# Optimization experiments

Measured on AMD Instinct MI355X. Metric: run time of the kernel, lower is better.

## Reference

```python
import jax, jax.numpy as jnp
import numpy as np

LN_EPS = 1e-5   # torch nn.LayerNorm default
R_EPS = 1e-8    # eps used in log(R.clamp(min=eps))


def layernorm(x, g, b):
    mu = jnp.mean(x, axis=-1, keepdims=True)
    var = jnp.var(x, axis=-1, keepdims=True)
    return (x - mu) * jax.lax.rsqrt(var + LN_EPS) * g + b


def setup_inputs() -> dict:
    S, B, C, h, w, d = 4, 1, 128, 10, 10, 10
    nL = 2  # num_layers
    key = jax.random.key(0)
    ks = jax.random.split(key, 20)
    std = 0.02
    inp = {
        "z": jax.random.normal(ks[0], (S, B, C, h, w, d), jnp.float32),
        "r": jax.random.uniform(ks[1], (S,), jnp.float32, 0.1, 1.0),
        "seq_embed": std * jax.random.normal(ks[2], (S, C), jnp.float32),
        # per-layer attention params, stacked on leading layer axis
        "Wq": std * jax.random.normal(ks[3], (nL, C, C), jnp.float32),
        "Wk": std * jax.random.normal(ks[4], (nL, C, C), jnp.float32),
        "Wv": std * jax.random.normal(ks[5], (nL, C, C), jnp.float32),
        "Wp": std * jax.random.normal(ks[6], (nL, C, C), jnp.float32),
        "beta": jnp.ones((nL,), jnp.float32),
        "ln1_g": jnp.ones((nL, C), jnp.float32),
        "ln1_b": jnp.zeros((nL, C), jnp.float32),
        # FFN params
        "ffn_w1": std * jax.random.normal(ks[7], (C, 4 * C), jnp.float32),
        "ffn_b1": jnp.zeros((4 * C,), jnp.float32),
        "ffn_w2": std * jax.random.normal(ks[8], (4 * C, C), jnp.float32),
        "ffn_b2": jnp.zeros((C,), jnp.float32),
        "ln2_g": jnp.ones((C,), jnp.float32),
        "ln2_b": jnp.zeros((C,), jnp.float32),
    }
    return inp


def _forward(z, r, seq_embed, Wq, Wk, Wv, Wp, beta, ln1_g, ln1_b,
             ffn_w1, ffn_b1, ffn_w2, ffn_b2, ln2_g, ln2_b):
    S, B, C, h, w, d = z.shape
    N = h * w * d
    L = S * N
    nL, _, _ = Wq.shape
    H = 8
    Dh = C // H
    scale = Dh ** (-0.5)

    # tokenize: [S,B,C,h,w,d] -> [B, S*N, C] with per-sequence embedding added
    tokens = z.reshape(S, B, C, N).transpose(1, 0, 3, 2)      # [B,S,N,C]
    tokens = tokens + seq_embed[None, :, None, :]
    tokens = tokens.reshape(B, L, C)

    # reliability bias: log(clamp(outer(r_tok, r_tok), eps))  [L,L]
    r_tok = jnp.repeat(r, N)                                   # [L]
    log_R = jnp.log(jnp.clip(r_tok[:, None] * r_tok[None, :], R_EPS, None))

    for l in range(nL):
        residual = tokens
        Q = (tokens @ Wq[l]).reshape(B, L, H, Dh)
        K = (tokens @ Wk[l]).reshape(B, L, H, Dh)
        V = (tokens @ Wv[l]).reshape(B, L, H, Dh)
        attn = jnp.einsum('bihd,bjhd->bhij', Q, K) * scale     # [B,H,L,L]
        attn = attn + beta[l] * log_R[None, None]
        attn = jax.nn.softmax(attn, axis=-1)
        out = jnp.einsum('bhij,bjhd->bihd', attn, V).reshape(B, L, C)
        out = out @ Wp[l]
        tokens = layernorm(out + residual, ln1_g[l], ln1_b[l])

    # FFN (exact GELU, matching torch nn.GELU default) + residual + LN
    hdn = jax.nn.gelu(tokens @ ffn_w1 + ffn_b1, approximate=False)
    tokens = layernorm((hdn @ ffn_w2 + ffn_b2) + tokens, ln2_g, ln2_b)

    # de-tokenize: [B,L,C] -> [B, S*C, h, w, d]
    tokens = tokens.reshape(B, S, N, C).transpose(0, 1, 3, 2)  # [B,S,C,N]
    return tokens.reshape(B, S * C, h, w, d)


def reference(z, r, seq_embed, Wq, Wk, Wv, Wp, beta, ln1_g, ln1_b,
              ffn_w1, ffn_b1, ffn_w2, ffn_b2, ln2_g, ln2_b):
    return _forward(z, r, seq_embed, Wq, Wk, Wv, Wp, beta, ln1_g, ln1_b,
                    ffn_w1, ffn_b1, ffn_w2, ffn_b2, ln2_g, ln2_b)
```

## Files before the change

kernel.cpp:

```cpp
#include <hip/hip_runtime.h>
#include <hip/hip_bf16.h>
#include <math.h>

#define LL 4000
#define CC 128
#define NN 1000
#define NLAYER 2
#define KSPLIT 4
#define SCLOG2 0.36067376022224085f
#define KROW 20
#define VROW 36

typedef __attribute__((ext_vector_type(4))) short bf16x4;
typedef __attribute__((ext_vector_type(8))) short short8;
typedef __attribute__((ext_vector_type(4))) float f32x4;
typedef __attribute__((ext_vector_type(2))) unsigned int u32x2;

__device__ __forceinline__ short bf16rne(float f) {
    return __builtin_bit_cast(short, __float2bfloat16(f));
}
__device__ __forceinline__ float bf16tof(short s) {
    return __builtin_bit_cast(float, (unsigned)((unsigned short)s) << 16);
}

__device__ __forceinline__ bf16x4 pack4(const float* p) {
    unsigned w01 = __builtin_amdgcn_perm(__builtin_bit_cast(unsigned, p[1]),
                                         __builtin_bit_cast(unsigned, p[0]),
                                         0x07060302u);
    unsigned w23 = __builtin_amdgcn_perm(__builtin_bit_cast(unsigned, p[3]),
                                         __builtin_bit_cast(unsigned, p[2]),
                                         0x07060302u);
    u32x2 w = {w01, w23};
    return __builtin_bit_cast(bf16x4, w);
}

__global__ void tokenize_kernel(const float* __restrict__ z,
                                const float* __restrict__ se,
                                float* __restrict__ tok,
                                short* __restrict__ tokb) {
    __shared__ float tl[32][33];
    const int s  = blockIdx.z;
    const int c0 = blockIdx.y * 32;
    const int n0 = blockIdx.x * 32;
    const int tx = threadIdx.x & 31, ty = threadIdx.x >> 5;
    #pragma unroll
    for (int i = 0; i < 4; ++i) {
        int n = n0 + tx;
        if (n < NN) tl[ty * 4 + i][tx] = z[((size_t)s * CC + c0 + ty * 4 + i) * NN + n];
    }
    __syncthreads();
    #pragma unroll
    for (int i = 0; i < 4; ++i) {
        int n = n0 + ty * 4 + i;
        if (n < NN) {
            int c = c0 + tx;
            float v = tl[tx][ty * 4 + i] + se[s * CC + c];
            size_t o = ((size_t)(s * NN + n)) * CC + c;
            tok[o] = v;
            tokb[o] = bf16rne(v);
        }
    }
}

__global__ void detok_kernel(const float* __restrict__ tok,
                             float* __restrict__ out) {
    __shared__ float tl[32][33];
    const int s  = blockIdx.z;
    const int c0 = blockIdx.y * 32;
    const int n0 = blockIdx.x * 32;
    const int tx = threadIdx.x & 31, ty = threadIdx.x >> 5;
    #pragma unroll
    for (int i = 0; i < 4; ++i) {
        int n = n0 + ty * 4 + i;
        if (n < NN) tl[ty * 4 + i][tx] = tok[((size_t)(s * NN + n)) * CC + c0 + tx];
    }
    __syncthreads();
    #pragma unroll
    for (int i = 0; i < 4; ++i) {
        int n = n0 + tx;
        if (n < NN) out[((size_t)s * CC + c0 + ty * 4 + i) * NN + n] = tl[tx][ty * 4 + i];
    }
}

__global__ void prep_weights(const float* __restrict__ Wq, const float* __restrict__ Wk,
                             const float* __restrict__ Wv, const float* __restrict__ Wp,
                             const float* __restrict__ w1, const float* __restrict__ w2,
                             const float* __restrict__ r, const float* __restrict__ beta,
                             short* __restrict__ wt8, short* __restrict__ w1t,
                             short* __restrict__ w2t, float* __restrict__ kbw) {
    int idx = blockIdx.x * blockDim.x + threadIdx.x;
    if (idx < 8 * 16384) {
        int m = idx >> 14, i = idx & 16383;
        int n = i >> 7, k = i & 127;
        const float* src = (m < 2) ? Wq + (size_t)m * 16384
                         : (m < 4) ? Wk + (size_t)(m - 2) * 16384
                         : (m < 6) ? Wv + (size_t)(m - 4) * 16384
                                   : Wp + (size_t)(m - 6) * 16384;
        wt8[idx] = bf16rne(src[k * 128 + n]);
    } else if (idx < 8 * 16384 + 65536) {
        int i = idx - 8 * 16384;
        int n = i >> 7, k = i & 127;
        w1t[i] = bf16rne(w1[(size_t)k * 512 + n]);
    } else if (idx < 8 * 16384 + 2 * 65536) {
        int i = idx - 8 * 16384 - 65536;
        int n = i >> 9, k = i & 511;
        w2t[i] = bf16rne(w2[(size_t)k * 128 + n]);
    } else if (idx < 8 * 16384 + 2 * 65536 + NLAYER * KSPLIT) {
        int i = idx - (8 * 16384 + 2 * 65536);
        int l = i / KSPLIT, zz = i - l * KSPLIT;
        kbw[i] = exp2f(beta[l] * __log2f(r[zz]));
    }
}

__device__ __forceinline__ void gemm_body(
        const short* __restrict__ A, const short* __restrict__ Wt,
        const float* __restrict__ bias, void* __restrict__ outp,
        int M, int K, int N, int flags, int row0, int col0) {
    __shared__ short Al[16][136];
    __shared__ short Wl[128][136];
    const int tid = threadIdx.x;
    const int lane = tid & 63;
    const int w = tid >> 6;
    const int lq = lane & 15, g = lane >> 4;

    f32x4 acc[2] = {{0.f,0.f,0.f,0.f},{0.f,0.f,0.f,0.f}};

    for (int kc = 0; kc < K; kc += 128) {
        {
            int r = tid >> 4, c = (tid & 15) * 8;
            *(short8*)&Al[r][c] = *(const short8*)(A + (size_t)(row0 + r) * K + kc + c);
        }
        {
            int c = (tid & 15) * 8;
            int nb = tid >> 4;
            #pragma unroll
            for (int i = 0; i < 8; ++i) {
                int n = nb + i * 16;
                *(short8*)&Wl[n][c] = *(const short8*)(Wt + (size_t)(col0 + n) * K + kc + c);
            }
        }
        __syncthreads();
        bf16x4 af[8];
        #pragma unroll
        for (int ks = 0; ks < 8; ++ks)
            af[ks] = *(const bf16x4*)&Al[lq][ks * 16 + g * 4];
        #pragma unroll
        for (int ct = 0; ct < 2; ++ct) {
            int n = (w * 2 + ct) * 16 + lq;
            #pragma unroll
            for (int ks = 0; ks < 8; ++ks) {
                bf16x4 bfr = *(const bf16x4*)&Wl[n][ks * 16 + g * 4];
                acc[ct] = __builtin_amdgcn_mfma_f32_16x16x16bf16_1k(af[ks], bfr, acc[ct], 0, 0, 0);
            }
        }
        __syncthreads();
    }
    #pragma unroll
    for (int ct = 0; ct < 2; ++ct) {
        int col = col0 + (w * 2 + ct) * 16 + lq;
        float bv = bias ? bias[col] : 0.f;
        float v[4];
        #pragma unroll
        for (int r = 0; r < 4; ++r) {
            v[r] = acc[ct][r] + bv;
            if (flags & 2) v[r] = 0.5f * v[r] * (1.f + erff(v[r] * 0.70710678118654752f));
            if (flags & 8) v[r] *= SCLOG2;
        }
        if (flags & 4) {
            bf16x4 res = {bf16rne(v[0]), bf16rne(v[1]), bf16rne(v[2]), bf16rne(v[3])};
            *(bf16x4*)((short*)outp + (size_t)col * M + row0 + g * 4) = res;
        } else if (flags & 16) {
            #pragma unroll
            for (int r = 0; r < 4; ++r)
                ((short*)outp)[((size_t)(col >> 4) * M + (row0 + g * 4 + r)) * 16 + (col & 15)] = bf16rne(v[r]);
        } else if (flags & 1) {
            #pragma unroll
            for (int r = 0; r < 4; ++r)
                ((short*)outp)[(size_t)(row0 + g * 4 + r) * N + col] = bf16rne(v[r]);
        } else {
            #pragma unroll
            for (int r = 0; r < 4; ++r)
                ((float*)outp)[(size_t)(row0 + g * 4 + r) * N + col] = v[r];
        }
    }
}

__global__ __launch_bounds__(256) void mfma_gemm(
        const short* __restrict__ A, const short* __restrict__ Wt,
        const float* __restrict__ bias, void* __restrict__ outp,
        int M, int K, int N, int flags) {
    gemm_body(A, Wt, bias, outp, M, K, N, flags,
              blockIdx.x * 16, blockIdx.y * 128);
}

__global__ __launch_bounds__(256) void mfma_gemm3(
        const short* __restrict__ A,
        const short* __restrict__ W0, const short* __restrict__ W1,
        const short* __restrict__ W2,
        short* __restrict__ o0, short* __restrict__ o1, short* __restrict__ o2,
        int M, int K, int N) {
    const short* Wt = (blockIdx.z == 0) ? W0 : (blockIdx.z == 1) ? W1 : W2;
    short* o = (blockIdx.z == 0) ? o0 : (blockIdx.z == 1) ? o1 : o2;
    int flags = (blockIdx.z == 0) ? (1 | 8) : (blockIdx.z == 1) ? 16 : 4;
    gemm_body(A, Wt, nullptr, o, M, K, N, flags, blockIdx.x * 16, 0);
}

__global__ __launch_bounds__(256) void mfma_gemm_ln(
        const short* __restrict__ A, const short* __restrict__ Wt,
        const float* __restrict__ bias, const float* __restrict__ resid,
        const float* __restrict__ gam, const float* __restrict__ bet,
        float* __restrict__ outf, short* __restrict__ outb,
        int M, int K) {
    __shared__ short Al[16][136];
    __shared__ short Wl[128][136];
    __shared__ float sL[4][4][4], s2L[4][4][4];
    const int tid = threadIdx.x;
    const int lane = tid & 63;
    const int w = tid >> 6;
    const int lq = lane & 15, g = lane >> 4;
    const int row0 = blockIdx.x * 16;

    f32x4 acc[2] = {{0.f,0.f,0.f,0.f},{0.f,0.f,0.f,0.f}};

    for (int kc = 0; kc < K; kc += 128) {
        {
            int r = tid >> 4, c = (tid & 15) * 8;
            *(short8*)&Al[r][c] = *(const short8*)(A + (size_t)(row0 + r) * K + kc + c);
        }
        {
            int c = (tid & 15) * 8;
            int nb = tid >> 4;
            #pragma unroll
            for (int i = 0; i < 8; ++i) {
                int n = nb + i * 16;
                *(short8*)&Wl[n][c] = *(const short8*)(Wt + (size_t)n * K + kc + c);
            }
        }
        __syncthreads();
        bf16x4 af[8];
        #pragma unroll
        for (int ks = 0; ks < 8; ++ks)
            af[ks] = *(const bf16x4*)&Al[lq][ks * 16 + g * 4];
        #pragma unroll
        for (int ct = 0; ct < 2; ++ct) {
            int n = (w * 2 + ct) * 16 + lq;
            #pragma unroll
            for (int ks = 0; ks < 8; ++ks) {
                bf16x4 bfr = *(const bf16x4*)&Wl[n][ks * 16 + g * 4];
                acc[ct] = __builtin_amdgcn_mfma_f32_16x16x16bf16_1k(af[ks], bfr, acc[ct], 0, 0, 0);
            }
        }
        __syncthreads();
    }

    float v[2][4];
    int cols[2] = {(w * 2) * 16 + lq, (w * 2 + 1) * 16 + lq};
    #pragma unroll
    for (int ct = 0; ct < 2; ++ct) {
        float bv = bias ? bias[cols[ct]] : 0.f;
        #pragma unroll
        for (int r = 0; r < 4; ++r)
            v[ct][r] = acc[ct][r] + bv +
                       resid[(size_t)(row0 + g * 4 + r) * CC + cols[ct]];
    }
    float sr[4], s2r[4];
    #pragma unroll
    for (int r = 0; r < 4; ++r) {
        sr[r]  = v[0][r] + v[1][r];
        s2r[r] = v[0][r] * v[0][r] + v[1][r] * v[1][r];
    }
    #pragma unroll
    for (int off = 1; off < 16; off <<= 1) {
        #pragma unroll
        for (int r = 0; r < 4; ++r) {
            sr[r]  += __shfl_xor(sr[r],  off);
            s2r[r] += __shfl_xor(s2r[r], off);
        }
    }
    if (lq == 0) {
        #pragma unroll
        for (int r = 0; r < 4; ++r) { sL[w][g][r] = sr[r]; s2L[w][g][r] = s2r[r]; }
    }
    __syncthreads();
    #pragma unroll
    for (int r = 0; r < 4; ++r) {
        float s = 0.f, s2 = 0.f;
        #pragma unroll
        for (int ww = 0; ww < 4; ++ww) { s += sL[ww][g][r]; s2 += s2L[ww][g][r]; }
        float mu = s * (1.f / CC);
        float var = s2 * (1.f / CC) - mu * mu;
        float rstd = rsqrtf(var + 1e-5f);
        size_t rowoff = (size_t)(row0 + g * 4 + r) * CC;
        #pragma unroll
        for (int ct = 0; ct < 2; ++ct) {
            float y = (v[ct][r] - mu) * rstd * gam[cols[ct]] + bet[cols[ct]];
            outf[rowoff + cols[ct]] = y;
            outb[rowoff + cols[ct]] = bf16rne(y);
        }
    }
}

__global__ __launch_bounds__(256) void mfma_gemm_ln_cmb(
        const short* __restrict__ pob, const float* __restrict__ pl,
        const short* __restrict__ Wt, const float* __restrict__ resid,
        const float* __restrict__ gam, const float* __restrict__ bet,
        float* __restrict__ outf, short* __restrict__ outb) {
    __shared__ short Al[16][136];
    __shared__ short Wl[128][136];
    __shared__ float sL[4][4][4], s2L[4][4][4];
    const int tid = threadIdx.x;
    const int lane = tid & 63;
    const int w = tid >> 6;
    const int lq = lane & 15, g = lane >> 4;
    const int row0 = blockIdx.x * 16;

    {
        int r = tid >> 4, c0 = (tid & 15) * 8;
        int row = row0 + r;
        int h = c0 >> 4;
        float a8[8] = {0.f,0.f,0.f,0.f,0.f,0.f,0.f,0.f};
        float den = 0.f;
        #pragma unroll
        for (int zz = 0; zz < KSPLIT; ++zz) {
            short8 t = *(const short8*)(pob + (size_t)zz * LL * CC + (size_t)row * CC + c0);
            #pragma unroll
            for (int j = 0; j < 8; ++j) a8[j] += bf16tof(t[j]);
            den += pl[(zz * 8 + h) * LL + row];
        }
        float inv = 1.f / den;
        short8 packed;
        #pragma unroll
        for (int j = 0; j < 8; ++j) packed[j] = bf16rne(a8[j] * inv);
        *(short8*)&Al[r][c0] = packed;
    }
    {
        int c = (tid & 15) * 8;
        int nb = tid >> 4;
        #pragma unroll
        for (int i = 0; i < 8; ++i) {
            int n = nb + i * 16;
            *(short8*)&Wl[n][c] = *(const short8*)(Wt + (size_t)n * CC + c);
        }
    }
    __syncthreads();

    f32x4 acc[2] = {{0.f,0.f,0.f,0.f},{0.f,0.f,0.f,0.f}};
    bf16x4 af[8];
    #pragma unroll
    for (int ks = 0; ks < 8; ++ks)
        af[ks] = *(const bf16x4*)&Al[lq][ks * 16 + g * 4];
    #pragma unroll
    for (int ct = 0; ct < 2; ++ct) {
        int n = (w * 2 + ct) * 16 + lq;
        #pragma unroll
        for (int ks = 0; ks < 8; ++ks) {
            bf16x4 bfr = *(const bf16x4*)&Wl[n][ks * 16 + g * 4];
            acc[ct] = __builtin_amdgcn_mfma_f32_16x16x16bf16_1k(af[ks], bfr, acc[ct], 0, 0, 0);
        }
    }

    float v[2][4];
    int cols[2] = {(w * 2) * 16 + lq, (w * 2 + 1) * 16 + lq};
    #pragma unroll
    for (int ct = 0; ct < 2; ++ct) {
        #pragma unroll
        for (int r = 0; r < 4; ++r)
            v[ct][r] = acc[ct][r] +
                       resid[(size_t)(row0 + g * 4 + r) * CC + cols[ct]];
    }
    float sr[4], s2r[4];
    #pragma unroll
    for (int r = 0; r < 4; ++r) {
        sr[r]  = v[0][r] + v[1][r];
        s2r[r] = v[0][r] * v[0][r] + v[1][r] * v[1][r];
    }
    #pragma unroll
    for (int off = 1; off < 16; off <<= 1) {
        #pragma unroll
        for (int r = 0; r < 4; ++r) {
            sr[r]  += __shfl_xor(sr[r],  off);
            s2r[r] += __shfl_xor(s2r[r], off);
        }
    }
    if (lq == 0) {
        #pragma unroll
        for (int r = 0; r < 4; ++r) { sL[w][g][r] = sr[r]; s2L[w][g][r] = s2r[r]; }
    }
    __syncthreads();
    #pragma unroll
    for (int r = 0; r < 4; ++r) {
        float s = 0.f, s2 = 0.f;
        #pragma unroll
        for (int ww = 0; ww < 4; ++ww) { s += sL[ww][g][r]; s2 += s2L[ww][g][r]; }
        float mu = s * (1.f / CC);
        float var = s2 * (1.f / CC) - mu * mu;
        float rstd = rsqrtf(var + 1e-5f);
        size_t rowoff = (size_t)(row0 + g * 4 + r) * CC;
        #pragma unroll
        for (int ct = 0; ct < 2; ++ct) {
            float y = (v[ct][r] - mu) * rstd * gam[cols[ct]] + bet[cols[ct]];
            outf[rowoff + cols[ct]] = y;
            outb[rowoff + cols[ct]] = bf16rne(y);
        }
    }
}

__global__ __launch_bounds__(256) void attn_mfma_kernel(
        const short* __restrict__ Qb, const short* __restrict__ Kh,
        const short* __restrict__ Vt, const float* __restrict__ kbw,
        short* __restrict__ pob, float* __restrict__ pl) {
    __shared__ short Kl[2][32][KROW];
    __shared__ short Vl[2][16][VROW];
    const int tid  = threadIdx.x;
    const int lane = tid & 63;
    const int wv   = tid >> 6;
    const int lq = lane & 15;
    const int g  = lane >> 4;
    const int h  = blockIdx.y;
    const int z  = blockIdx.z;
    const int qtA = blockIdx.x * 8 + wv * 2;
    const int qtB = qtA + 1;
    const bool qvA = qtA < LL / 16;
    const bool qvB = qtB < LL / 16;
    const int hd0 = h * 16;
    const int kbase = z * NN;

    bf16x4 qfA = {0, 0, 0, 0}, qfB = {0, 0, 0, 0};
    if (qvA) qfA = *(const bf16x4*)(Qb + (size_t)(qtA * 16 + lq) * CC + hd0 + 4 * g);
    if (qvB) qfB = *(const bf16x4*)(Qb + (size_t)(qtB * 16 + lq) * CC + hd0 + 4 * g);

    const short onev = (lq == 0) ? (short)0x3F80 : (short)0;
    const bf16x4 af1 = {onev, onev, onev, onev};

    const short* kgp = Kh + ((size_t)h * LL + kbase) * 16 + tid * 2;
    const short* vgp = Vt + (size_t)(hd0 + (tid >> 4)) * LL + kbase + (tid & 15) * 2;
    short* kwp = &Kl[0][0][0] + (tid >> 3) * KROW + (tid & 7) * 2;
    short* vwp = &Vl[0][0][0] + (tid >> 4) * VROW + (tid & 15) * 2;
    const int kbufstride = 32 * KROW;
    const int vbufstride = 16 * VROW;

    f32x4 oA  = {0.f, 0.f, 0.f, 0.f}, oB  = {0.f, 0.f, 0.f, 0.f};
    f32x4 psA = {0.f, 0.f, 0.f, 0.f}, psB = {0.f, 0.f, 0.f, 0.f};

    {
        unsigned kd = *(const unsigned*)kgp;
        unsigned vd = *(const unsigned*)vgp;
        *(unsigned*)kwp = kd;
        *(unsigned*)vwp = vd;
    }
    unsigned kdA = *(const unsigned*)(kgp + (size_t)32 * 16);
    unsigned vdA = *(const unsigned*)(vgp + 32);
    __syncthreads();

    for (int t = 0; t < 31; ++t) {
        unsigned kdB, vdB;
        if (t < 30) {
            kdB = *(const unsigned*)(kgp + (size_t)(t + 2) * 32 * 16);
            vdB = *(const unsigned*)(vgp + (t + 2) * 32);
        }

        {
            const short* kb = &Kl[t & 1][0][0];
            const short* vb = &Vl[t & 1][0][0];
            bf16x4 K0 = *(const bf16x4*)(kb + lq * KROW + 4 * g);
            bf16x4 K1 = *(const bf16x4*)(kb + (16 + lq) * KROW + 4 * g);
            bf16x4 V0 = *(const bf16x4*)(vb + lq * VROW + 4 * g);
            bf16x4 V1 = *(const bf16x4*)(vb + lq * VROW + 16 + 4 * g);
            const f32x4 zz = {0.f, 0.f, 0.f, 0.f};
            f32x4 sA0 = __builtin_amdgcn_mfma_f32_16x16x16bf16_1k(K0, qfA, zz, 0, 0, 0);
            f32x4 sA1 = __builtin_amdgcn_mfma_f32_16x16x16bf16_1k(K1, qfA, zz, 0, 0, 0);
            f32x4 sB0 = __builtin_amdgcn_mfma_f32_16x16x16bf16_1k(K0, qfB, zz, 0, 0, 0);
            f32x4 sB1 = __builtin_amdgcn_mfma_f32_16x16x16bf16_1k(K1, qfB, zz, 0, 0, 0);
            float pA0[4], pA1[4], pB0[4], pB1[4];
            #pragma unroll
            for (int r = 0; r < 4; ++r) {
                pA0[r] = __builtin_amdgcn_exp2f(sA0[r]);
                pA1[r] = __builtin_amdgcn_exp2f(sA1[r]);
                pB0[r] = __builtin_amdgcn_exp2f(sB0[r]);
                pB1[r] = __builtin_amdgcn_exp2f(sB1[r]);
            }
            bf16x4 ptA0 = pack4(pA0), ptA1 = pack4(pA1);
            bf16x4 ptB0 = pack4(pB0), ptB1 = pack4(pB1);
            oA  = __builtin_amdgcn_mfma_f32_16x16x16bf16_1k(V0, ptA0, oA, 0, 0, 0);
            oA  = __builtin_amdgcn_mfma_f32_16x16x16bf16_1k(V1, ptA1, oA, 0, 0, 0);
            oB  = __builtin_amdgcn_mfma_f32_16x16x16bf16_1k(V0, ptB0, oB, 0, 0, 0);
            oB  = __builtin_amdgcn_mfma_f32_16x16x16bf16_1k(V1, ptB1, oB, 0, 0, 0);
            psA = __builtin_amdgcn_mfma_f32_16x16x16bf16_1k(af1, ptA0, psA, 0, 0, 0);
            psA = __builtin_amdgcn_mfma_f32_16x16x16bf16_1k(af1, ptA1, psA, 0, 0, 0);
            psB = __builtin_amdgcn_mfma_f32_16x16x16bf16_1k(af1, ptB0, psB, 0, 0, 0);
            psB = __builtin_amdgcn_mfma_f32_16x16x16bf16_1k(af1, ptB1, psB, 0, 0, 0);
        }

        const int nb = (t + 1) & 1;
        *(unsigned*)(kwp + nb * kbufstride) = kdA;
        *(unsigned*)(vwp + nb * vbufstride) = vdA;
        __syncthreads();
        if (t < 30) { kdA = kdB; vdA = vdB; }
    }

    {
        const short* kb = &Kl[1][0][0];
        const short* vb = &Vl[1][0][0];
        bf16x4 K0 = *(const bf16x4*)(kb + lq * KROW + 4 * g);
        bf16x4 V0 = *(const bf16x4*)(vb + lq * VROW + 4 * g);
        if (g >= 2) V0 = (bf16x4){0, 0, 0, 0};
        const f32x4 zz = {0.f, 0.f, 0.f, 0.f};
        f32x4 sA0 = __builtin_amdgcn_mfma_f32_16x16x16bf16_1k(K0, qfA, zz, 0, 0, 0);
        f32x4 sB0 = __builtin_amdgcn_mfma_f32_16x16x16bf16_1k(K0, qfB, zz, 0, 0, 0);
        float pA0[4], pB0[4];
        #pragma unroll
        for (int r = 0; r < 4; ++r) {
            pA0[r] = (g < 2) ? __builtin_amdgcn_exp2f(sA0[r]) : 0.f;
            pB0[r] = (g < 2) ? __builtin_amdgcn_exp2f(sB0[r]) : 0.f;
        }
        bf16x4 ptA0 = pack4(pA0), ptB0 = pack4(pB0);
        oA  = __builtin_amdgcn_mfma_f32_16x16x16bf16_1k(V0, ptA0, oA, 0, 0, 0);
        oB  = __builtin_amdgcn_mfma_f32_16x16x16bf16_1k(V0, ptB0, oB, 0, 0, 0);
        psA = __builtin_amdgcn_mfma_f32_16x16x16bf16_1k(af1, ptA0, psA, 0, 0, 0);
        psB = __builtin_amdgcn_mfma_f32_16x16x16bf16_1k(af1, ptB0, psB, 0, 0, 0);
    }

    const float wz = kbw[z];
    if (qvA) {
        bf16x4 ow = {bf16rne(oA[0] * wz), bf16rne(oA[1] * wz),
                     bf16rne(oA[2] * wz), bf16rne(oA[3] * wz)};
        *(bf16x4*)(pob + (size_t)z * LL * CC + (size_t)(qtA * 16 + lq) * CC + hd0 + 4 * g) = ow;
        if (g == 0) pl[(z * 8 + h) * LL + qtA * 16 + lq] = psA[0] * wz;
    }
    if (qvB) {
        bf16x4 ow = {bf16rne(oB[0] * wz), bf16rne(oB[1] * wz),
                     bf16rne(oB[2] * wz), bf16rne(oB[3] * wz)};
        *(bf16x4*)(pob + (size_t)z * LL * CC + (size_t)(qtB * 16 + lq) * CC + hd0 + 4 * g) = ow;
        if (g == 0) pl[(z * 8 + h) * LL + qtB * 16 + lq] = psB[0] * wz;
    }
}

extern "C" void kernel_launch(void* const* d_in, const int* in_sizes, int n_in,
                              void* d_out, int out_size, void* d_ws, size_t ws_size,
                              hipStream_t stream) {
    const float* z    = (const float*)d_in[0];
    const float* r    = (const float*)d_in[1];
    const float* se   = (const float*)d_in[2];
    const float* Wq   = (const float*)d_in[3];
    const float* Wk   = (const float*)d_in[4];
    const float* Wv   = (const float*)d_in[5];
    const float* Wp   = (const float*)d_in[6];
    const float* beta = (const float*)d_in[7];
    const float* ln1g = (const float*)d_in[8];
    const float* ln1b = (const float*)d_in[9];
    const float* w1   = (const float*)d_in[10];
    const float* b1   = (const float*)d_in[11];
    const float* w2   = (const float*)d_in[12];
    const float* b2   = (const float*)d_in[13];
    const float* ln2g = (const float*)d_in[14];
    const float* ln2b = (const float*)d_in[15];
    float* out = (float*)d_out;

    float* ws   = (float*)d_ws;
    float* tok  = ws;
    float* kbw  = tok + LL * CC;
    float* pl   = kbw + 8;
    short* pob  = (short*)(pl + KSPLIT * 8 * LL);
    short* hdn  = pob;
    short* tokb = pob + (size_t)KSPLIT * LL * CC;
    short* Qb   = tokb + LL * CC;
    short* Kh   = Qb   + LL * CC;
    short* Vt   = Kh   + LL * CC + 1024;
    short* wt8  = Vt   + LL * CC + 1024;
    short* w1t  = wt8  + 8 * 16384;
    short* w2t  = w1t  + 65536;

    prep_weights<<<1025, 256, 0, stream>>>(Wq, Wk, Wv, Wp, w1, w2, r, beta,
                                           wt8, w1t, w2t, kbw);
    tokenize_kernel<<<dim3(32, 4, 4), 256, 0, stream>>>(z, se, tok, tokb);

    for (int l = 0; l < NLAYER; ++l) {
        const short* wqt = wt8 + (size_t)(0 * 2 + l) * 16384;
        const short* wkt = wt8 + (size_t)(1 * 2 + l) * 16384;
        const short* wvt = wt8 + (size_t)(2 * 2 + l) * 16384;
        const short* wpt = wt8 + (size_t)(3 * 2 + l) * 16384;
        mfma_gemm3<<<dim3(LL / 16, 1, 3), 256, 0, stream>>>(
            tokb, wqt, wkt, wvt, Qb, Kh, Vt, LL, CC, CC);
        attn_mfma_kernel<<<dim3((LL / 16 + 7) / 8, 8, KSPLIT), 256, 0, stream>>>(
            Qb, Kh, Vt, kbw + l * KSPLIT, pob, pl);
        mfma_gemm_ln_cmb<<<LL / 16, 256, 0, stream>>>(
            pob, pl, wpt, tok, ln1g + l * CC, ln1b + l * CC, tok, tokb);
    }

    mfma_gemm<<<dim3(LL / 16, 4), 256, 0, stream>>>(tokb, w1t, b1, hdn, LL, CC, 4 * CC, 1 | 2);
    mfma_gemm_ln<<<LL / 16, 256, 0, stream>>>(
        hdn, w2t, b2, tok, ln2g, ln2b, tok, tokb, LL, 4 * CC);

    detok_kernel<<<dim3(32, 4, 4), 256, 0, stream>>>(tok, out);
}
```

Baseline: 100.2 us.

## Fuse FFN GEMMs into one kernel and merge weight prep with tokenize

The two FFN GEMMs (W1 with GELU, then W2 with residual and LayerNorm) are combined into a single kernel. Each 16-row block keeps its 512-wide hidden activation in shared memory instead of writing it to global memory and reading it back. Separately, weight conversion and tokenization now run in one launch through block-index dispatch, saving a kernel launch. The cost is more shared memory per block (an extra ~16KB buffer), which may reduce occupancy, and the FFN now has only 250 blocks where the W1 GEMM previously had 1000.

```diff
diff --git a/kernel.cpp b/kernel.cpp
--- a/kernel.cpp
+++ b/kernel.cpp
@@ -34,30 +34,61 @@
     return __builtin_bit_cast(bf16x4, w);
 }
 
-__global__ void tokenize_kernel(const float* __restrict__ z,
-                                const float* __restrict__ se,
-                                float* __restrict__ tok,
-                                short* __restrict__ tokb) {
+__global__ void prep_tok_kernel(const float* __restrict__ Wq, const float* __restrict__ Wk,
+                                const float* __restrict__ Wv, const float* __restrict__ Wp,
+                                const float* __restrict__ w1, const float* __restrict__ w2,
+                                const float* __restrict__ r, const float* __restrict__ beta,
+                                short* __restrict__ wt8, short* __restrict__ w1t,
+                                short* __restrict__ w2t, float* __restrict__ kbw,
+                                const float* __restrict__ z, const float* __restrict__ se,
+                                float* __restrict__ tok, short* __restrict__ tokb) {
     __shared__ float tl[32][33];
-    const int s  = blockIdx.z;
-    const int c0 = blockIdx.y * 32;
-    const int n0 = blockIdx.x * 32;
-    const int tx = threadIdx.x & 31, ty = threadIdx.x >> 5;
-    #pragma unroll
-    for (int i = 0; i < 4; ++i) {
-        int n = n0 + tx;
-        if (n < NN) tl[ty * 4 + i][tx] = z[((size_t)s * CC + c0 + ty * 4 + i) * NN + n];
-    }
-    __syncthreads();
-    #pragma unroll
-    for (int i = 0; i < 4; ++i) {
-        int n = n0 + ty * 4 + i;
-        if (n < NN) {
-            int c = c0 + tx;
-            float v = tl[tx][ty * 4 + i] + se[s * CC + c];
-            size_t o = ((size_t)(s * NN + n)) * CC + c;
-            tok[o] = v;
-            tokb[o] = bf16rne(v);
+    const int bid = blockIdx.x;
+    if (bid < 1025) {
+        int idx = bid * 256 + threadIdx.x;
+        if (idx < 8 * 16384) {
+            int m = idx >> 14, i = idx & 16383;
+            int n = i >> 7, k = i & 127;
+            const float* src = (m < 2) ? Wq + (size_t)m * 16384
+                             : (m < 4) ? Wk + (size_t)(m - 2) * 16384
+                             : (m < 6) ? Wv + (size_t)(m - 4) * 16384
+                                       : Wp + (size_t)(m - 6) * 16384;
+            wt8[idx] = bf16rne(src[k * 128 + n]);
+        } else if (idx < 8 * 16384 + 65536) {
+            int i = idx - 8 * 16384;
+            int n = i >> 7, k = i & 127;
+            w1t[i] = bf16rne(w1[(size_t)k * 512 + n]);
+        } else if (idx < 8 * 16384 + 2 * 65536) {
+            int i = idx - 8 * 16384 - 65536;
+            int n = i >> 9, k = i & 511;
+            w2t[i] = bf16rne(w2[(size_t)k * 128 + n]);
+        } else if (idx < 8 * 16384 + 2 * 65536 + NLAYER * KSPLIT) {
+            int i = idx - (8 * 16384 + 2 * 65536);
+            int l = i / KSPLIT, zz = i - l * KSPLIT;
+            kbw[i] = exp2f(beta[l] * __log2f(r[zz]));
+        }
+    } else {
+        int b2 = bid - 1025;
+        const int n0 = (b2 & 31) * 32;
+        const int c0 = ((b2 >> 5) & 3) * 32;
+        const int s  = b2 >> 7;
+        const int tx = threadIdx.x & 31, ty = threadIdx.x >> 5;
+        #pragma unroll
+        for (int i = 0; i < 4; ++i) {
+            int n = n0 + tx;
+            if (n < NN) tl[ty * 4 + i][tx] = z[((size_t)s * CC + c0 + ty * 4 + i) * NN + n];
+        }
+        __syncthreads();
+        #pragma unroll
+        for (int i = 0; i < 4; ++i) {
+            int n = n0 + ty * 4 + i;
+            if (n < NN) {
+                int c = c0 + tx;
+                float v = tl[tx][ty * 4 + i] + se[s * CC + c];
+                size_t o = ((size_t)(s * NN + n)) * CC + c;
+                tok[o] = v;
+                tokb[o] = bf16rne(v);
+            }
         }
     }
 }
@@ -79,36 +110,6 @@
     for (int i = 0; i < 4; ++i) {
         int n = n0 + tx;
         if (n < NN) out[((size_t)s * CC + c0 + ty * 4 + i) * NN + n] = tl[tx][ty * 4 + i];
-    }
-}
-
-__global__ void prep_weights(const float* __restrict__ Wq, const float* __restrict__ Wk,
-                             const float* __restrict__ Wv, const float* __restrict__ Wp,
-                             const float* __restrict__ w1, const float* __restrict__ w2,
-                             const float* __restrict__ r, const float* __restrict__ beta,
-                             short* __restrict__ wt8, short* __restrict__ w1t,
-                             short* __restrict__ w2t, float* __restrict__ kbw) {
-    int idx = blockIdx.x * blockDim.x + threadIdx.x;
-    if (idx < 8 * 16384) {
-        int m = idx >> 14, i = idx & 16383;
-        int n = i >> 7, k = i & 127;
-        const float* src = (m < 2) ? Wq + (size_t)m * 16384
-                         : (m < 4) ? Wk + (size_t)(m - 2) * 16384
-                         : (m < 6) ? Wv + (size_t)(m - 4) * 16384
-                                   : Wp + (size_t)(m - 6) * 16384;
-        wt8[idx] = bf16rne(src[k * 128 + n]);
-    } else if (idx < 8 * 16384 + 65536) {
-        int i = idx - 8 * 16384;
-        int n = i >> 7, k = i & 127;
-        w1t[i] = bf16rne(w1[(size_t)k * 512 + n]);
-    } else if (idx < 8 * 16384 + 2 * 65536) {
-        int i = idx - 8 * 16384 - 65536;
-        int n = i >> 9, k = i & 511;
-        w2t[i] = bf16rne(w2[(size_t)k * 128 + n]);
-    } else if (idx < 8 * 16384 + 2 * 65536 + NLAYER * KSPLIT) {
-        int i = idx - (8 * 16384 + 2 * 65536);
-        int l = i / KSPLIT, zz = i - l * KSPLIT;
-        kbw[i] = exp2f(beta[l] * __log2f(r[zz]));
     }
 }
 
@@ -185,14 +186,6 @@
     }
 }
 
-__global__ __launch_bounds__(256) void mfma_gemm(
-        const short* __restrict__ A, const short* __restrict__ Wt,
-        const float* __restrict__ bias, void* __restrict__ outp,
-        int M, int K, int N, int flags) {
-    gemm_body(A, Wt, bias, outp, M, K, N, flags,
-              blockIdx.x * 16, blockIdx.y * 128);
-}
-
 __global__ __launch_bounds__(256) void mfma_gemm3(
         const short* __restrict__ A,
         const short* __restrict__ W0, const short* __restrict__ W1,
@@ -203,101 +196,6 @@
     short* o = (blockIdx.z == 0) ? o0 : (blockIdx.z == 1) ? o1 : o2;
     int flags = (blockIdx.z == 0) ? (1 | 8) : (blockIdx.z == 1) ? 16 : 4;
     gemm_body(A, Wt, nullptr, o, M, K, N, flags, blockIdx.x * 16, 0);
-}
-
-__global__ __launch_bounds__(256) void mfma_gemm_ln(
-        const short* __restrict__ A, const short* __restrict__ Wt,
-        const float* __restrict__ bias, const float* __restrict__ resid,
-        const float* __restrict__ gam, const float* __restrict__ bet,
-        float* __restrict__ outf, short* __restrict__ outb,
-        int M, int K) {
-    __shared__ short Al[16][136];
-    __shared__ short Wl[128][136];
-    __shared__ float sL[4][4][4], s2L[4][4][4];
-    const int tid = threadIdx.x;
-    const int lane = tid & 63;
-    const int w = tid >> 6;
-    const int lq = lane & 15, g = lane >> 4;
-    const int row0 = blockIdx.x * 16;
-
-    f32x4 acc[2] = {{0.f,0.f,0.f,0.f},{0.f,0.f,0.f,0.f}};
-
-    for (int kc = 0; kc < K; kc += 128) {
-        {
-            int r = tid >> 4, c = (tid & 15) * 8;
-            *(short8*)&Al[r][c] = *(const short8*)(A + (size_t)(row0 + r) * K + kc + c);
-        }
-        {
-            int c = (tid & 15) * 8;
-            int nb = tid >> 4;
-            #pragma unroll
-            for (int i = 0; i < 8; ++i) {
-                int n = nb + i * 16;
-                *(short8*)&Wl[n][c] = *(const short8*)(Wt + (size_t)n * K + kc + c);
-            }
-        }
-        __syncthreads();
-        bf16x4 af[8];
-        #pragma unroll
-        for (int ks = 0; ks < 8; ++ks)
-            af[ks] = *(const bf16x4*)&Al[lq][ks * 16 + g * 4];
-        #pragma unroll
-        for (int ct = 0; ct < 2; ++ct) {
-            int n = (w * 2 + ct) * 16 + lq;
-            #pragma unroll
-            for (int ks = 0; ks < 8; ++ks) {
-                bf16x4 bfr = *(const bf16x4*)&Wl[n][ks * 16 + g * 4];
-                acc[ct] = __builtin_amdgcn_mfma_f32_16x16x16bf16_1k(af[ks], bfr, acc[ct], 0, 0, 0);
-            }
-        }
-        __syncthreads();
-    }
-
-    float v[2][4];
-    int cols[2] = {(w * 2) * 16 + lq, (w * 2 + 1) * 16 + lq};
-    #pragma unroll
-    for (int ct = 0; ct < 2; ++ct) {
-        float bv = bias ? bias[cols[ct]] : 0.f;
-        #pragma unroll
-        for (int r = 0; r < 4; ++r)
-            v[ct][r] = acc[ct][r] + bv +
-                       resid[(size_t)(row0 + g * 4 + r) * CC + cols[ct]];
-    }
-    float sr[4], s2r[4];
-    #pragma unroll
-    for (int r = 0; r < 4; ++r) {
-        sr[r]  = v[0][r] + v[1][r];
-        s2r[r] = v[0][r] * v[0][r] + v[1][r] * v[1][r];
-    }
-    #pragma unroll
-    for (int off = 1; off < 16; off <<= 1) {
-        #pragma unroll
-        for (int r = 0; r < 4; ++r) {
-            sr[r]  += __shfl_xor(sr[r],  off);
-            s2r[r] += __shfl_xor(s2r[r], off);
-        }
-    }
-    if (lq == 0) {
-        #pragma unroll
-        for (int r = 0; r < 4; ++r) { sL[w][g][r] = sr[r]; s2L[w][g][r] = s2r[r]; }
-    }
-    __syncthreads();
-    #pragma unroll
-    for (int r = 0; r < 4; ++r) {
-        float s = 0.f, s2 = 0.f;
-        #pragma unroll
-        for (int ww = 0; ww < 4; ++ww) { s += sL[ww][g][r]; s2 += s2L[ww][g][r]; }
-        float mu = s * (1.f / CC);
-        float var = s2 * (1.f / CC) - mu * mu;
-        float rstd = rsqrtf(var + 1e-5f);
-        size_t rowoff = (size_t)(row0 + g * 4 + r) * CC;
-        #pragma unroll
-        for (int ct = 0; ct < 2; ++ct) {
-            float y = (v[ct][r] - mu) * rstd * gam[cols[ct]] + bet[cols[ct]];
-            outf[rowoff + cols[ct]] = y;
-            outb[rowoff + cols[ct]] = bf16rne(y);
-        }
-    }
 }
 
 __global__ __launch_bounds__(256) void mfma_gemm_ln_cmb(
@@ -366,6 +264,143 @@
         #pragma unroll
         for (int r = 0; r < 4; ++r)
             v[ct][r] = acc[ct][r] +
+                       resid[(size_t)(row0 + g * 4 + r) * CC + cols[ct]];
+    }
+    float sr[4], s2r[4];
+    #pragma unroll
+    for (int r = 0; r < 4; ++r) {
+        sr[r]  = v[0][r] + v[1][r];
+        s2r[r] = v[0][r] * v[0][r] + v[1][r] * v[1][r];
+    }
+    #pragma unroll
+    for (int off = 1; off < 16; off <<= 1) {
+        #pragma unroll
+        for (int r = 0; r < 4; ++r) {
+            sr[r]  += __shfl_xor(sr[r],  off);
+            s2r[r] += __shfl_xor(s2r[r], off);
+        }
+    }
+    if (lq == 0) {
+        #pragma unroll
+        for (int r = 0; r < 4; ++r) { sL[w][g][r] = sr[r]; s2L[w][g][r] = s2r[r]; }
+    }
+    __syncthreads();
+    #pragma unroll
+    for (int r = 0; r < 4; ++r) {
+        float s = 0.f, s2 = 0.f;
+        #pragma unroll
+        for (int ww = 0; ww < 4; ++ww) { s += sL[ww][g][r]; s2 += s2L[ww][g][r]; }
+        float mu = s * (1.f / CC);
+        float var = s2 * (1.f / CC) - mu * mu;
+        float rstd = rsqrtf(var + 1e-5f);
+        size_t rowoff = (size_t)(row0 + g * 4 + r) * CC;
+        #pragma unroll
+        for (int ct = 0; ct < 2; ++ct) {
+            float y = (v[ct][r] - mu) * rstd * gam[cols[ct]] + bet[cols[ct]];
+            outf[rowoff + cols[ct]] = y;
+            outb[rowoff + cols[ct]] = bf16rne(y);
+        }
+    }
+}
+
+__global__ __launch_bounds__(256) void fused_ffn(
+        const short* __restrict__ tokb, const short* __restrict__ w1t,
+        const float* __restrict__ b1, const short* __restrict__ w2t,
+        const float* __restrict__ b2, const float* __restrict__ resid,
+        const float* __restrict__ gam, const float* __restrict__ bet,
+        float* __restrict__ outf, short* __restrict__ outb) {
+    __shared__ short Al[16][136];
+    __shared__ short Wl[128][136];
+    __shared__ short Hl[16][520];
+    __shared__ float sL[4][4][4], s2L[4][4][4];
+    const int tid = threadIdx.x;
+    const int lane = tid & 63;
+    const int w = tid >> 6;
+    const int lq = lane & 15, g = lane >> 4;
+    const int row0 = blockIdx.x * 16;
+
+    {
+        int r = tid >> 4, c = (tid & 15) * 8;
+        *(short8*)&Al[r][c] = *(const short8*)(tokb + (size_t)(row0 + r) * CC + c);
+    }
+
+    bf16x4 af[8];
+    for (int cc = 0; cc < 4; ++cc) {
+        {
+            int c = (tid & 15) * 8;
+            int nb = tid >> 4;
+            #pragma unroll
+            for (int i = 0; i < 8; ++i) {
+                int n = nb + i * 16;
+                *(short8*)&Wl[n][c] = *(const short8*)(w1t + (size_t)(cc * 128 + n) * CC + c);
+            }
+        }
+        __syncthreads();
+        if (cc == 0) {
+            #pragma unroll
+            for (int ks = 0; ks < 8; ++ks)
+                af[ks] = *(const bf16x4*)&Al[lq][ks * 16 + g * 4];
+        }
+        f32x4 acc[2] = {{0.f,0.f,0.f,0.f},{0.f,0.f,0.f,0.f}};
+        #pragma unroll
+        for (int ct = 0; ct < 2; ++ct) {
+            int n = (w * 2 + ct) * 16 + lq;
+            #pragma unroll
+            for (int ks = 0; ks < 8; ++ks) {
+                bf16x4 bfr = *(const bf16x4*)&Wl[n][ks * 16 + g * 4];
+                acc[ct] = __builtin_amdgcn_mfma_f32_16x16x16bf16_1k(af[ks], bfr, acc[ct], 0, 0, 0);
+            }
+        }
+        #pragma unroll
+        for (int ct = 0; ct < 2; ++ct) {
+            int col = (w * 2 + ct) * 16 + lq;
+            float bv = b1[cc * 128 + col];
+            #pragma unroll
+            for (int r = 0; r < 4; ++r) {
+                float v = acc[ct][r] + bv;
+                v = 0.5f * v * (1.f + erff(v * 0.70710678118654752f));
+                Hl[g * 4 + r][cc * 128 + col] = bf16rne(v);
+            }
+        }
+        __syncthreads();
+    }
+
+    f32x4 acc2[2] = {{0.f,0.f,0.f,0.f},{0.f,0.f,0.f,0.f}};
+    for (int kc = 0; kc < 4; ++kc) {
+        {
+            int c = (tid & 15) * 8;
+            int nb = tid >> 4;
+            #pragma unroll
+            for (int i = 0; i < 8; ++i) {
+                int n = nb + i * 16;
+                *(short8*)&Wl[n][c] = *(const short8*)(w2t + (size_t)n * 512 + kc * 128 + c);
+            }
+        }
+        __syncthreads();
+        bf16x4 hf[8];
+        #pragma unroll
+        for (int ks = 0; ks < 8; ++ks)
+            hf[ks] = *(const bf16x4*)&Hl[lq][kc * 128 + ks * 16 + g * 4];
+        #pragma unroll
+        for (int ct = 0; ct < 2; ++ct) {
+            int n = (w * 2 + ct) * 16 + lq;
+            #pragma unroll
+            for (int ks = 0; ks < 8; ++ks) {
+                bf16x4 bfr = *(const bf16x4*)&Wl[n][ks * 16 + g * 4];
+                acc2[ct] = __builtin_amdgcn_mfma_f32_16x16x16bf16_1k(hf[ks], bfr, acc2[ct], 0, 0, 0);
+            }
+        }
+        __syncthreads();
+    }
+
+    float v[2][4];
+    int cols[2] = {(w * 2) * 16 + lq, (w * 2 + 1) * 16 + lq};
+    #pragma unroll
+    for (int ct = 0; ct < 2; ++ct) {
+        float bv = b2[cols[ct]];
+        #pragma unroll
+        for (int r = 0; r < 4; ++r)
+            v[ct][r] = acc2[ct][r] + bv +
                        resid[(size_t)(row0 + g * 4 + r) * CC + cols[ct]];
     }
     float sr[4], s2r[4];
@@ -458,7 +493,6 @@
             kdB = *(const unsigned*)(kgp + (size_t)(t + 2) * 32 * 16);
             vdB = *(const unsigned*)(vgp + (t + 2) * 32);
         }
-
         {
             const short* kb = &Kl[t & 1][0][0];
             const short* vb = &Vl[t & 1][0][0];
@@ -490,7 +524,6 @@
             psB = __builtin_amdgcn_mfma_f32_16x16x16bf16_1k(af1, ptB0, psB, 0, 0, 0);
             psB = __builtin_amdgcn_mfma_f32_16x16x16bf16_1k(af1, ptB1, psB, 0, 0, 0);
         }
-
         const int nb = (t + 1) & 1;
         *(unsigned*)(kwp + nb * kbufstride) = kdA;
         *(unsigned*)(vwp + nb * vbufstride) = vdA;
@@ -561,7 +594,6 @@
     float* kbw  = tok + LL * CC;
     float* pl   = kbw + 8;
     short* pob  = (short*)(pl + KSPLIT * 8 * LL);
-    short* hdn  = pob;
     short* tokb = pob + (size_t)KSPLIT * LL * CC;
     short* Qb   = tokb + LL * CC;
     short* Kh   = Qb   + LL * CC;
@@ -570,9 +602,8 @@
     short* w1t  = wt8  + 8 * 16384;
     short* w2t  = w1t  + 65536;
 
-    prep_weights<<<1025, 256, 0, stream>>>(Wq, Wk, Wv, Wp, w1, w2, r, beta,
-                                           wt8, w1t, w2t, kbw);
-    tokenize_kernel<<<dim3(32, 4, 4), 256, 0, stream>>>(z, se, tok, tokb);
+    prep_tok_kernel<<<1537, 256, 0, stream>>>(Wq, Wk, Wv, Wp, w1, w2, r, beta,
+                                              wt8, w1t, w2t, kbw, z, se, tok, tokb);
 
     for (int l = 0; l < NLAYER; ++l) {
         const short* wqt = wt8 + (size_t)(0 * 2 + l) * 16384;
@@ -587,9 +618,8 @@
             pob, pl, wpt, tok, ln1g + l * CC, ln1b + l * CC, tok, tokb);
     }
 
-    mfma_gemm<<<dim3(LL / 16, 4), 256, 0, stream>>>(tokb, w1t, b1, hdn, LL, CC, 4 * CC, 1 | 2);
-    mfma_gemm_ln<<<LL / 16, 256, 0, stream>>>(
-        hdn, w2t, b2, tok, ln2g, ln2b, tok, tokb, LL, 4 * CC);
+    fused_ffn<<<LL / 16, 256, 0, stream>>>(
+        tokb, w1t, b1, w2t, b2, tok, ln2g, ln2b, tok, tokb);
 
     detok_kernel<<<dim3(32, 4, 4), 256, 0, stream>>>(tok, out);
 }
```

Result: faster. 94.61 us (-5.5%).
